# Kernel optimization log

Measured on AMD Instinct MI355X. Metric: run time of the kernel, lower is better.

Reference implementation:

```python
import jax, jax.numpy as jnp
import numpy as np

N, E, D, H, O = 50000, 800000, 128, 256, 64
BN_EPS = 1e-5


def setup_inputs() -> dict:
    key = jax.random.key(0)
    ks = jax.random.split(key, 12)
    x_indices = jnp.arange(N, dtype=jnp.int64) if jax.config.jax_enable_x64 else jnp.arange(N, dtype=jnp.int32)
    ei = jax.random.randint(ks[0], (2, E), 0, N, dtype=jnp.int32)
    s = lambda k, shape, fan: jax.random.normal(k, shape, dtype=jnp.float32) * (1.0 / np.sqrt(fan))
    return {
        "x_indices": x_indices,
        "ei": ei,
        "emb": jax.random.normal(ks[1], (N, D), dtype=jnp.float32),
        "W1": s(ks[2], (D, H), D), "b1": jnp.zeros((H,), jnp.float32),
        "g1": jnp.ones((H,), jnp.float32), "be1": jnp.zeros((H,), jnp.float32),
        "W2": s(ks[3], (H, H), H), "b2": jnp.zeros((H,), jnp.float32),
        "g2": jnp.ones((H,), jnp.float32), "be2": jnp.zeros((H,), jnp.float32),
        "W3": s(ks[4], (H, O), H), "b3": jnp.zeros((O,), jnp.float32),
    }


def reference(x_indices, ei, emb, W1, b1, g1, be1, W2, b2, g2, be2, W3, b3):
    n = emb.shape[0]
    # GCN normalization with self-loops (PyG GCNConv default):
    loop = jnp.arange(n, dtype=ei.dtype)
    row = jnp.concatenate([ei[0], loop])  # source
    col = jnp.concatenate([ei[1], loop])  # target (aggregation index)
    deg = jax.ops.segment_sum(jnp.ones_like(col, dtype=emb.dtype), col, num_segments=n)
    dinv = jnp.where(deg > 0, 1.0 / jnp.sqrt(jnp.maximum(deg, 1.0)), 0.0)
    norm = dinv[row] * dinv[col]  # [E+N]

    def conv(x, W, b):
        xl = x @ W                                   # [N, d_out]
        msg = xl[row] * norm[:, None]                # gather + scale
        return jax.ops.segment_sum(msg, col, num_segments=n) + b  # scatter-add

    def bn(x, g, be):  # batch-stat BatchNorm1d (training-mode stats)
        m = jnp.mean(x, axis=0)
        v = jnp.var(x, axis=0)
        return (x - m) * (g / jnp.sqrt(v + BN_EPS)) + be

    x = emb[x_indices]
    x = jax.nn.relu(bn(conv(x, W1, b1), g1, be1))
    x = jax.nn.relu(bn(conv(x, W2, b2), g2, be2))
    return conv(x, W3, b3)
```

## Files before the change

### kernel.cpp

```cpp
#include <hip/hip_runtime.h>
#include <hip/hip_bf16.h>

#define Dk 128
#define Hk 256
#define Ok 64
#define BN_EPS 1e-5f
#define NSLICE 8

typedef __attribute__((ext_vector_type(8))) short short8;
typedef __attribute__((ext_vector_type(4))) float f32x4;

static __device__ __forceinline__ float bf2f(ushort u) {
    union { uint32_t i; float f; } c; c.i = ((uint32_t)u) << 16; return c.f;
}
static __device__ __forceinline__ ushort f2bf(float f) {
    union { float f; uint32_t u; } c; c.f = f;
    return (ushort)((c.u + 0x7fffu + ((c.u >> 16) & 1u)) >> 16);
}


#define W1SZ (Dk * Hk)
#define W2SZ (Hk * Hk)
#define W3SZ (Hk * Ok)
#define WBLK ((W1SZ + W2SZ + W3SZ) / 256)
#define STATSP_FLOATS (2 * NSLICE * 512)

__global__ void count_cvt_kernel(const int* __restrict__ ecol, int* __restrict__ cnt, int E,
                                 const float* __restrict__ emb, const int* __restrict__ xidx,
                                 ushort* __restrict__ embb,
                                 const float* __restrict__ W1, const float* __restrict__ W2,
                                 const float* __restrict__ W3, ushort* __restrict__ W1t,
                                 ushort* __restrict__ W2t, ushort* __restrict__ W3t,
                                 float* __restrict__ statsP, int n) {
    const int cntBlocks = (E + 255) >> 8;
    const int embBlocks = (n * (Dk / 8) + 255) >> 8;
    int bid = blockIdx.x;
    if (bid < cntBlocks) {
        int e = bid * 256 + threadIdx.x;
        if (e < E) atomicAdd(&cnt[ecol[e]], 1);
        return;
    }
    bid -= cntBlocks;
    if (bid < embBlocks) {
        int gid = bid * 256 + threadIdx.x;
        int total = n * (Dk / 8);
        if (gid >= total) return;
        int node = gid >> 4, seg = gid & 15;
        int src = xidx[node];
        const float* p = &emb[(size_t)src * Dk + seg * 8];
        float4 lo = *(const float4*)p, hi = *(const float4*)(p + 4);
        ushort r[8] = {f2bf(lo.x), f2bf(lo.y), f2bf(lo.z), f2bf(lo.w),
                       f2bf(hi.x), f2bf(hi.y), f2bf(hi.z), f2bf(hi.w)};
        *(short8*)&embb[(size_t)gid * 8] = *(short8*)r;
        return;
    }
    bid -= embBlocks;
    if (bid < WBLK) {
        int gid = bid * 256 + threadIdx.x;
        if (gid < W1SZ) {
            int c = gid / Dk, k = gid - c * Dk;
            W1t[gid] = f2bf(W1[(size_t)k * Hk + c]);
        } else if (gid < W1SZ + W2SZ) {
            int idx = gid - W1SZ;
            int c = idx / Hk, k = idx - c * Hk;
            W2t[idx] = f2bf(W2[(size_t)k * Hk + c]);
        } else {
            int idx = gid - W1SZ - W2SZ;
            int c = idx / Hk, k = idx - c * Hk;
            W3t[idx] = f2bf(W3[(size_t)k * Ok + c]);
        }
        return;
    }
    bid -= WBLK;
    int idx = bid * 1024 + threadIdx.x * 4;
    if (idx < STATSP_FLOATS)
        *(float4*)&statsP[idx] = make_float4(0.f, 0.f, 0.f, 0.f);
}

__global__ void dinv_bsum_kernel(const int* __restrict__ cnt, float* __restrict__ dinv,
                                 int* __restrict__ fillc, int* __restrict__ bsum, int n) {
    __shared__ int sm[256];
    int i = blockIdx.x * 256 + threadIdx.x;
    int c = (i < n) ? cnt[i] : 0;
    if (i < n) { dinv[i] = rsqrtf((float)c + 1.0f); fillc[i] = 0; }
    sm[threadIdx.x] = c;
    __syncthreads();
    for (int s = 128; s; s >>= 1) {
        if (threadIdx.x < s) sm[threadIdx.x] += sm[threadIdx.x + s];
        __syncthreads();
    }
    if (!threadIdx.x) bsum[blockIdx.x] = sm[0];
}

__global__ void scan_off_kernel(const int* __restrict__ cnt, const int* __restrict__ bsum,
                                int* __restrict__ offv, int n) {
    __shared__ int sm[256];
    __shared__ int sbase;
    int t = threadIdx.x, bidx = blockIdx.x;
    int part = 0;
    for (int j = t; j < bidx; j += 256) part += bsum[j];
    sm[t] = part;
    __syncthreads();
    for (int s = 128; s; s >>= 1) {
        if (t < s) sm[t] += sm[t + s];
        __syncthreads();
    }
    if (t == 0) sbase = sm[0];
    __syncthreads();
    int base = sbase;
    __syncthreads();
    int i = bidx * 256 + t;
    int v = (i < n) ? cnt[i] : 0;
    sm[t] = v;
    __syncthreads();
    for (int s = 1; s < 256; s <<= 1) {
        int add = (t >= s) ? sm[t - s] : 0;
        __syncthreads();
        sm[t] += add;
        __syncthreads();
    }
    if (i < n) offv[i + 1] = base + sm[t];
    if (i == 0) offv[0] = 0;
}

__global__ void fill_kernel(const int* __restrict__ row, const int* __restrict__ col,
                            const int* __restrict__ off, int* __restrict__ fillc,
                            const float* __restrict__ dinv, int2* __restrict__ ep, int E) {
    int e = blockIdx.x * blockDim.x + threadIdx.x;
    if (e < E) {
        int c = col[e], r = row[e];
        int p = atomicAdd(&fillc[c], 1);
        ep[off[c] + p] = make_int2(r, __float_as_int(dinv[r]));
    }
}

__global__ void bn_finalize_kernel(const float* __restrict__ statsP, const float* __restrict__ g,
                                   const float* __restrict__ be, float* __restrict__ ss,
                                   float invn) {
    int f = threadIdx.x;
    float sum = 0.f, sq = 0.f;
    #pragma unroll
    for (int s = 0; s < NSLICE; ++s) {
        sum += statsP[s * 512 + f];
        sq  += statsP[s * 512 + 256 + f];
    }
    float mean = sum * invn;
    float var = sq * invn - mean * mean;
    float sc = g[f] * rsqrtf(var + BN_EPS);
    ss[f] = sc;
    ss[256 + f] = fmaf(-mean, sc, be[f]);
}


template<int KD, int BNT, bool STATS, bool BIAS, bool BN_A>
__global__ __launch_bounds__(256) void gemm128(
    const ushort* __restrict__ A, const ushort* __restrict__ Wt,
    ushort* __restrict__ Cout, int n, int Hout,
    const float* __restrict__ bias, float* __restrict__ statsP,
    const float* __restrict__ ss)
{
    constexpr int WN = (BNT == 128) ? 2 : 1;
    constexpr int MR = (BNT == 128) ? 4 : 2;
    constexpr int NR = 4;
    constexpr int TILE = (128 + BNT) * 32;
    constexpr int NT = KD / 32;
    __shared__ ushort lds[2 * TILE];
    __shared__ float ssc[BN_A ? KD : 1];
    __shared__ float ssh[BN_A ? KD : 1];

    const int tid = threadIdx.x;
    const int lane = tid & 63, wid = tid >> 6;
    const int wr = wid / WN, wc = wid % WN;
    const int lr = lane & 15, lg = lane >> 4;
    const int bm = blockIdx.x * 128;
    const int bn = blockIdx.y * BNT;

    if (BN_A) {
        for (int f = tid; f < KD; f += 256) {
            ssc[f] = ss[f];
            ssh[f] = ss[KD + f];
        }
        __syncthreads();
    }

    auto stage = [&](int buf, int k0) {
        ushort* As = lds + buf * TILE;
        ushort* Bs = As + 128 * 32;
        #pragma unroll
        for (int c = 0; c < 2; ++c) {
            int boff = wid * 2048 + c * 1024 + lane * 16;
            int row = boff >> 6;
            int k8 = (boff >> 4) & 3;
            int grow = bm + row; if (grow >= n) grow = n - 1;
            const ushort* src = &A[(size_t)grow * KD + k0 + k8 * 8];
            if (BN_A) {
                short8 av = *(const short8*)src;
                ushort r[8];
                #pragma unroll
                for (int j = 0; j < 8; ++j) {
                    int kf = k0 + k8 * 8 + j;
                    float v = bf2f((ushort)av[j]);
                    r[j] = f2bf(fmaxf(fmaf(v, ssc[kf], ssh[kf]), 0.f));
                }
                *(short8*)&As[row * 32 + k8 * 8] = *(short8*)r;
            } else {
                __builtin_amdgcn_global_load_lds(
                    (const __attribute__((address_space(1))) void*)src,
                    (__attribute__((address_space(3))) void*)&As[(wid * 2048 + c * 1024) >> 1],
                    16, 0, 0);
            }
        }
        constexpr int BC = BNT * 64 / 4096;
        #pragma unroll
        for (int c = 0; c < BC; ++c) {
            int boff = wid * (BNT * 16) + c * 1024 + lane * 16;
            int col = boff >> 6;
            int k8 = (boff >> 4) & 3;
            const ushort* src = &Wt[(size_t)(bn + col) * KD + k0 + k8 * 8];
            __builtin_amdgcn_global_load_lds(
                (const __attribute__((address_space(1))) void*)src,
                (__attribute__((address_space(3))) void*)&Bs[(wid * (BNT * 16) + c * 1024) >> 1],
                16, 0, 0);
        }
    };

    f32x4 acc[MR][NR] = {};

    stage(0, 0);
    __syncthreads();
    int cur = 0;
    for (int t = 0; t < NT; ++t) {
        if (t + 1 < NT) stage(cur ^ 1, (t + 1) * 32);
        ushort* As = lds + cur * TILE;
        ushort* Bs = As + 128 * 32;
        short8 af[MR], bfr[NR];
        #pragma unroll
        for (int m = 0; m < MR; ++m)
            af[m] = *(const short8*)&As[(wr * MR * 16 + m * 16 + lr) * 32 + lg * 8];
        #pragma unroll
        for (int nn = 0; nn < NR; ++nn)
            bfr[nn] = *(const short8*)&Bs[(wc * NR * 16 + nn * 16 + lr) * 32 + lg * 8];
        #pragma unroll
        for (int m = 0; m < MR; ++m)
            #pragma unroll
            for (int nn = 0; nn < NR; ++nn)
                acc[m][nn] = __builtin_amdgcn_mfma_f32_16x16x32_bf16(af[m], bfr[nn], acc[m][nn], 0, 0, 0);
        __syncthreads();
        cur ^= 1;
    }

    float s[NR], q[NR];
    #pragma unroll
    for (int nn = 0; nn < NR; ++nn) { s[nn] = 0.f; q[nn] = 0.f; }
    #pragma unroll
    for (int nn = 0; nn < NR; ++nn) {
        int col = bn + wc * NR * 16 + nn * 16 + lr;
        float bv = BIAS ? bias[col] : 0.f;
        #pragma unroll
        for (int m = 0; m < MR; ++m) {
            #pragma unroll
            for (int i = 0; i < 4; ++i) {
                int row = bm + wr * MR * 16 + m * 16 + lg * 4 + i;
                if (row < n) {
                    float v = acc[m][nn][i] + bv;
                    Cout[(size_t)row * Hout + col] = f2bf(v);
                    if (STATS) { s[nn] += v; q[nn] += v * v; }
                }
            }
        }
    }
    if (STATS) {
        float* sp = statsP + (size_t)(blockIdx.x & (NSLICE - 1)) * 2 * 256;
        #pragma unroll
        for (int nn = 0; nn < NR; ++nn) {
            s[nn] += __shfl_xor(s[nn], 16);
            q[nn] += __shfl_xor(q[nn], 16);
            s[nn] += __shfl_xor(s[nn], 32);
            q[nn] += __shfl_xor(q[nn], 32);
            if (lg == 0) {
                int col = bn + wc * NR * 16 + nn * 16 + lr;
                atomicAdd(&sp[col], s[nn]);
                atomicAdd(&sp[256 + col], q[nn]);
            }
        }
    }
}


template<int FH, int EPI, int MODE>
__global__ __launch_bounds__(256) void agg_kernel(
    const ushort* __restrict__ x, const int2* __restrict__ ep, const int* __restrict__ off,
    const float* __restrict__ dinv, const float* __restrict__ ss,
    const float* __restrict__ bias, void* __restrict__ outp, int n)
{
    constexpr int LPG = 64 / EPI;
    constexpr int VEC = FH / LPG;
    constexpr int U = 8 / EPI;
    const int tid = threadIdx.x;
    const int lane = tid & 63;
    const int wid = tid >> 6;
    const int node = blockIdx.x * 4 + wid;
    if (node >= n) return;
    const int grp = lane / LPG;
    const int flane = lane % LPG;
    const int fb = flane * VEC;
    const ushort* __restrict__ xb = x + fb;

    float sc[VEC], sh[VEC];
    if (MODE == 1) {
        float4 c4 = *(const float4*)&ss[fb];
        float4 h4 = *(const float4*)&ss[FH + fb];
        sc[0] = c4.x; sc[1] = c4.y; sc[2] = c4.z; sc[3] = c4.w;
        sh[0] = h4.x; sh[1] = h4.y; sh[2] = h4.z; sh[3] = h4.w;
    }
    auto xform = [&](ushort u, int v) -> float {
        float val = bf2f(u);
        if (MODE == 1) val = fmaxf(fmaf(val, sc[v], sh[v]), 0.f);
        return val;
    };

    float di = dinv[node];
    float acc[VEC] = {0.f, 0.f, 0.f, 0.f};
    if (EPI == 1 || grp == 0) {
        ushort4 t = *(const ushort4*)&xb[(size_t)node * FH];
        acc[0] = di * xform(t.x, 0); acc[1] = di * xform(t.y, 1);
        acc[2] = di * xform(t.z, 2); acc[3] = di * xform(t.w, 3);
    }
    const int e1 = off[node + 1];
    int b = off[node];
    for (; b + 8 <= e1; b += 8) {
        int2 p[U];
        ushort4 t[U];
        #pragma unroll
        for (int u = 0; u < U; ++u) p[u] = ep[b + grp + u * EPI];
        #pragma unroll
        for (int u = 0; u < U; ++u) t[u] = *(const ushort4*)&xb[(size_t)p[u].x * FH];
        #pragma unroll
        for (int u = 0; u < U; ++u) {
            float w = __int_as_float(p[u].y);
            acc[0] = fmaf(w, xform(t[u].x, 0), acc[0]);
            acc[1] = fmaf(w, xform(t[u].y, 1), acc[1]);
            acc[2] = fmaf(w, xform(t[u].z, 2), acc[2]);
            acc[3] = fmaf(w, xform(t[u].w, 3), acc[3]);
        }
    }
    if (b < e1) {
        #pragma unroll
        for (int u = 0; u < U; ++u) {
            int idx = b + grp + u * EPI;
            bool ok = idx < e1;
            int2 pp = ep[ok ? idx : b];
            ushort4 tt = *(const ushort4*)&xb[(size_t)pp.x * FH];
            float w = ok ? __int_as_float(pp.y) : 0.f;
            acc[0] = fmaf(w, xform(tt.x, 0), acc[0]);
            acc[1] = fmaf(w, xform(tt.y, 1), acc[1]);
            acc[2] = fmaf(w, xform(tt.z, 2), acc[2]);
            acc[3] = fmaf(w, xform(tt.w, 3), acc[3]);
        }
    }
    if (EPI == 4) {
        #pragma unroll
        for (int v = 0; v < VEC; ++v) acc[v] += __shfl_xor(acc[v], 16);
    }
    if (EPI >= 2) {
        #pragma unroll
        for (int v = 0; v < VEC; ++v) acc[v] += __shfl_xor(acc[v], 32);
    }
    if (grp == 0) {
        if (MODE == 2) {
            float4 bv = *(const float4*)&bias[fb];
            float4 res;
            res.x = fmaf(di, acc[0], bv.x); res.y = fmaf(di, acc[1], bv.y);
            res.z = fmaf(di, acc[2], bv.z); res.w = fmaf(di, acc[3], bv.w);
            *(float4*)((float*)outp + (size_t)node * FH + fb) = res;
        } else {
            ushort4 o;
            o.x = f2bf(di * acc[0]); o.y = f2bf(di * acc[1]);
            o.z = f2bf(di * acc[2]); o.w = f2bf(di * acc[3]);
            *(ushort4*)((ushort*)outp + (size_t)node * FH + fb) = o;
        }
    }
}


extern "C" void kernel_launch(void* const* d_in, const int* in_sizes, int n_in,
                              void* d_out, int out_size, void* d_ws, size_t ws_size,
                              hipStream_t stream) {
    const int*   x_idx = (const int*)d_in[0];
    const int*   ei    = (const int*)d_in[1];
    const float* emb   = (const float*)d_in[2];
    const float* W1    = (const float*)d_in[3];
    const float* b1    = (const float*)d_in[4];
    const float* g1    = (const float*)d_in[5];
    const float* be1   = (const float*)d_in[6];
    const float* W2    = (const float*)d_in[7];
    const float* b2    = (const float*)d_in[8];
    const float* g2    = (const float*)d_in[9];
    const float* be2   = (const float*)d_in[10];
    const float* W3    = (const float*)d_in[11];
    const float* b3    = (const float*)d_in[12];

    const int N = in_sizes[0];
    const int E = in_sizes[1] / 2;
    const int* erow = ei;
    const int* ecol = ei + E;

    char* p = (char*)d_ws;
    auto alloc = [&](size_t bytes) { char* q = p; p += (bytes + 255) & ~(size_t)255; return q; };
    const int nb = (N + 255) / 256;
    float*  dinv  = (float*) alloc((size_t)N * 4);
    int*    cnt   = (int*)   alloc((size_t)N * 4);
    int*    off   = (int*)   alloc((size_t)(N + 1) * 4);
    int*    fillc = (int*)   alloc((size_t)N * 4);
    int*    bsum  = (int*)   alloc((size_t)nb * 4);
    int2*   ep    = (int2*)  alloc((size_t)E * 8);
    float*  statsP= (float*) alloc((size_t)STATSP_FLOATS * 4);
    float*  stats1P = statsP, *stats2P = statsP + NSLICE * 512;
    float*  ss1   = (float*) alloc(512 * 4);
    float*  ss2   = (float*) alloc(512 * 4);
    ushort* W1t   = (ushort*)alloc((size_t)Dk * Hk * 2);
    ushort* W2t   = (ushort*)alloc((size_t)Hk * Hk * 2);
    ushort* W3t   = (ushort*)alloc((size_t)Hk * Ok * 2);
    ushort* bufU  = (ushort*)alloc((size_t)N * Hk * 2);
    ushort* embb  = bufU;
    ushort* agg1b = bufU + (size_t)N * Dk;
    ushort* conv2b= bufU;
    ushort* conv1b= (ushort*)alloc((size_t)N * Hk * 2);
    ushort* agg2b = (ushort*)alloc((size_t)N * Hk * 2);
    ushort* xl3b  = (ushort*)alloc((size_t)N * Ok * 2);

    const float invn = 1.0f / (float)N;

    hipMemsetAsync(cnt, 0, (size_t)N * 4, stream);
    const int cntBlocks = (E + 255) / 256;
    const int embBlocks = (N * (Dk / 8) + 255) / 256;
    count_cvt_kernel<<<cntBlocks + embBlocks + WBLK + (STATSP_FLOATS + 1023) / 1024,
                       256, 0, stream>>>(
        ecol, cnt, E, emb, x_idx, embb, W1, W2, W3, W1t, W2t, W3t, statsP, N);
    dinv_bsum_kernel<<<nb, 256, 0, stream>>>(cnt, dinv, fillc, bsum, N);
    scan_off_kernel<<<nb, 256, 0, stream>>>(cnt, bsum, off, N);
    fill_kernel<<<(E + 255) / 256, 256, 0, stream>>>(erow, ecol, off, fillc, dinv, ep, E);

    const int rb128 = (N + 127) / 128;
    const int aggBlocks = (N + 3) / 4;

    agg_kernel<Dk, 2, 0><<<aggBlocks, 256, 0, stream>>>(
        embb, ep, off, dinv, nullptr, nullptr, agg1b, N);
    gemm128<Dk, 128, true, true, false><<<dim3(rb128, Hk / 128), 256, 0, stream>>>(
        agg1b, W1t, conv1b, N, Hk, b1, stats1P, nullptr);
    bn_finalize_kernel<<<1, 256, 0, stream>>>(stats1P, g1, be1, ss1, invn);

    agg_kernel<Hk, 1, 1><<<aggBlocks, 256, 0, stream>>>(
        conv1b, ep, off, dinv, ss1, nullptr, agg2b, N);
    gemm128<Hk, 128, true, true, false><<<dim3(rb128, Hk / 128), 256, 0, stream>>>(
        agg2b, W2t, conv2b, N, Hk, b2, stats2P, nullptr);
    bn_finalize_kernel<<<1, 256, 0, stream>>>(stats2P, g2, be2, ss2, invn);

    gemm128<Hk, 64, false, false, true><<<dim3(rb128, 1), 256, 0, stream>>>(
        conv2b, W3t, xl3b, N, Ok, nullptr, nullptr, ss2);
    agg_kernel<Ok, 4, 2><<<aggBlocks, 256, 0, stream>>>(
        xl3b, ep, off, dinv, nullptr, b3, d_out, N);
}
```

Measured before the change: 300.5 us.

## Split BN statistics out of GEMM epilogue and tighten aggregation tail loop

Removes the per-block sum and sum-of-squares reduction and atomics from the GEMM epilogue, and computes BatchNorm statistics in a separate kernel that re-reads the bf16 conv output. This shrinks GEMM epilogue register pressure and atomic traffic, at the cost of an extra launch and a full extra read of the N×256 activation per layer. Statistics are now taken from bf16-rounded values rather than fp32 accumulators, which slightly changes numerics. The aggregation tail also replaces the masked 8-wide remainder with a 2×EPI unrolled loop plus a short masked loop, avoiding wasted gathers on nodes with few leftover edges.

```diff
diff --git a/kernel.cpp b/kernel.cpp
--- a/kernel.cpp
+++ b/kernel.cpp
@@ -134,6 +134,32 @@
     }
 }
 
+
+__global__ __launch_bounds__(256) void bn_stats_kernel(
+    const ushort* __restrict__ x, float* __restrict__ statsP, int n)
+{
+    __shared__ float red[8][256];
+    const int tid = threadIdx.x;
+    const int cg = tid & 63;
+    const int rg = tid >> 6;
+    const int c0 = cg * 4;
+    float s[4] = {0.f, 0.f, 0.f, 0.f}, q[4] = {0.f, 0.f, 0.f, 0.f};
+    for (int r = blockIdx.x * 4 + rg; r < n; r += gridDim.x * 4) {
+        ushort4 v = *(const ushort4*)&x[(size_t)r * Hk + c0];
+        float a0 = bf2f(v.x), a1 = bf2f(v.y), a2 = bf2f(v.z), a3 = bf2f(v.w);
+        s[0] += a0; s[1] += a1; s[2] += a2; s[3] += a3;
+        q[0] += a0 * a0; q[1] += a1 * a1; q[2] += a2 * a2; q[3] += a3 * a3;
+    }
+    #pragma unroll
+    for (int j = 0; j < 4; ++j) { red[rg][c0 + j] = s[j]; red[4 + rg][c0 + j] = q[j]; }
+    __syncthreads();
+    float ts = red[0][tid] + red[1][tid] + red[2][tid] + red[3][tid];
+    float tq = red[4][tid] + red[5][tid] + red[6][tid] + red[7][tid];
+    float* sp = statsP + (size_t)(blockIdx.x & (NSLICE - 1)) * 512;
+    atomicAdd(&sp[tid], ts);
+    atomicAdd(&sp[256 + tid], tq);
+}
+
 __global__ void bn_finalize_kernel(const float* __restrict__ statsP, const float* __restrict__ g,
                                    const float* __restrict__ be, float* __restrict__ ss,
                                    float invn) {
@@ -152,12 +178,11 @@
 }
 
 
-template<int KD, int BNT, bool STATS, bool BIAS, bool BN_A>
+template<int KD, int BNT, bool BIAS, bool BN_A>
 __global__ __launch_bounds__(256) void gemm128(
     const ushort* __restrict__ A, const ushort* __restrict__ Wt,
     ushort* __restrict__ Cout, int n, int Hout,
-    const float* __restrict__ bias, float* __restrict__ statsP,
-    const float* __restrict__ ss)
+    const float* __restrict__ bias, const float* __restrict__ ss)
 {
     constexpr int WN = (BNT == 128) ? 2 : 1;
     constexpr int MR = (BNT == 128) ? 4 : 2;
@@ -249,9 +274,6 @@
         cur ^= 1;
     }
 
-    float s[NR], q[NR];
-    #pragma unroll
-    for (int nn = 0; nn < NR; ++nn) { s[nn] = 0.f; q[nn] = 0.f; }
     #pragma unroll
     for (int nn = 0; nn < NR; ++nn) {
         int col = bn + wc * NR * 16 + nn * 16 + lr;
@@ -261,26 +283,8 @@
             #pragma unroll
             for (int i = 0; i < 4; ++i) {
                 int row = bm + wr * MR * 16 + m * 16 + lg * 4 + i;
-                if (row < n) {
-                    float v = acc[m][nn][i] + bv;
-                    Cout[(size_t)row * Hout + col] = f2bf(v);
-                    if (STATS) { s[nn] += v; q[nn] += v * v; }
-                }
-            }
-        }
-    }
-    if (STATS) {
-        float* sp = statsP + (size_t)(blockIdx.x & (NSLICE - 1)) * 2 * 256;
-        #pragma unroll
-        for (int nn = 0; nn < NR; ++nn) {
-            s[nn] += __shfl_xor(s[nn], 16);
-            q[nn] += __shfl_xor(q[nn], 16);
-            s[nn] += __shfl_xor(s[nn], 32);
-            q[nn] += __shfl_xor(q[nn], 32);
-            if (lg == 0) {
-                int col = bn + wc * NR * 16 + nn * 16 + lr;
-                atomicAdd(&sp[col], s[nn]);
-                atomicAdd(&sp[256 + col], q[nn]);
+                if (row < n)
+                    Cout[(size_t)row * Hout + col] = f2bf(acc[m][nn][i] + bv);
             }
         }
     }
@@ -344,19 +348,26 @@
             acc[3] = fmaf(w, xform(t[u].w, 3), acc[3]);
         }
     }
-    if (b < e1) {
-        #pragma unroll
-        for (int u = 0; u < U; ++u) {
-            int idx = b + grp + u * EPI;
-            bool ok = idx < e1;
-            int2 pp = ep[ok ? idx : b];
-            ushort4 tt = *(const ushort4*)&xb[(size_t)pp.x * FH];
-            float w = ok ? __int_as_float(pp.y) : 0.f;
-            acc[0] = fmaf(w, xform(tt.x, 0), acc[0]);
-            acc[1] = fmaf(w, xform(tt.y, 1), acc[1]);
-            acc[2] = fmaf(w, xform(tt.z, 2), acc[2]);
-            acc[3] = fmaf(w, xform(tt.w, 3), acc[3]);
-        }
+    if (EPI < 4) {
+        for (; b + 2 * EPI <= e1; b += 2 * EPI) {
+            int2 p0 = ep[b + grp], p1 = ep[b + grp + EPI];
+            ushort4 t0 = *(const ushort4*)&xb[(size_t)p0.x * FH];
+            ushort4 t1 = *(const ushort4*)&xb[(size_t)p1.x * FH];
+            float w0 = __int_as_float(p0.y), w1 = __int_as_float(p1.y);
+            acc[0] = fmaf(w0, xform(t0.x, 0), acc[0]); acc[1] = fmaf(w0, xform(t0.y, 1), acc[1]);
+            acc[2] = fmaf(w0, xform(t0.z, 2), acc[2]); acc[3] = fmaf(w0, xform(t0.w, 3), acc[3]);
+            acc[0] = fmaf(w1, xform(t1.x, 0), acc[0]); acc[1] = fmaf(w1, xform(t1.y, 1), acc[1]);
+            acc[2] = fmaf(w1, xform(t1.z, 2), acc[2]); acc[3] = fmaf(w1, xform(t1.w, 3), acc[3]);
+        }
+    }
+    for (; b < e1; b += EPI) {
+        int idx = b + grp;
+        bool ok = idx < e1;
+        int2 pp = ep[ok ? idx : e1 - 1];
+        ushort4 tt = *(const ushort4*)&xb[(size_t)pp.x * FH];
+        float w = ok ? __int_as_float(pp.y) : 0.f;
+        acc[0] = fmaf(w, xform(tt.x, 0), acc[0]); acc[1] = fmaf(w, xform(tt.y, 1), acc[1]);
+        acc[2] = fmaf(w, xform(tt.z, 2), acc[2]); acc[3] = fmaf(w, xform(tt.w, 3), acc[3]);
     }
     if (EPI == 4) {
         #pragma unroll
@@ -446,18 +457,20 @@
 
     agg_kernel<Dk, 2, 0><<<aggBlocks, 256, 0, stream>>>(
         embb, ep, off, dinv, nullptr, nullptr, agg1b, N);
-    gemm128<Dk, 128, true, true, false><<<dim3(rb128, Hk / 128), 256, 0, stream>>>(
-        agg1b, W1t, conv1b, N, Hk, b1, stats1P, nullptr);
+    gemm128<Dk, 128, true, false><<<dim3(rb128, Hk / 128), 256, 0, stream>>>(
+        agg1b, W1t, conv1b, N, Hk, b1, nullptr);
+    bn_stats_kernel<<<128, 256, 0, stream>>>(conv1b, stats1P, N);
     bn_finalize_kernel<<<1, 256, 0, stream>>>(stats1P, g1, be1, ss1, invn);
 
     agg_kernel<Hk, 1, 1><<<aggBlocks, 256, 0, stream>>>(
         conv1b, ep, off, dinv, ss1, nullptr, agg2b, N);
-    gemm128<Hk, 128, true, true, false><<<dim3(rb128, Hk / 128), 256, 0, stream>>>(
-        agg2b, W2t, conv2b, N, Hk, b2, stats2P, nullptr);
+    gemm128<Hk, 128, true, false><<<dim3(rb128, Hk / 128), 256, 0, stream>>>(
+        agg2b, W2t, conv2b, N, Hk, b2, nullptr);
+    bn_stats_kernel<<<128, 256, 0, stream>>>(conv2b, stats2P, N);
     bn_finalize_kernel<<<1, 256, 0, stream>>>(stats2P, g2, be2, ss2, invn);
 
-    gemm128<Hk, 64, false, false, true><<<dim3(rb128, 1), 256, 0, stream>>>(
-        conv2b, W3t, xl3b, N, Ok, nullptr, nullptr, ss2);
+    gemm128<Hk, 64, false, true><<<dim3(rb128, 1), 256, 0, stream>>>(
+        conv2b, W3t, xl3b, N, Ok, nullptr, ss2);
     agg_kernel<Ok, 4, 2><<<aggBlocks, 256, 0, stream>>>(
         xl3b, ep, off, dinv, nullptr, b3, d_out, N);
 }
```

New measurement: 338.6 us. +12.7%, slower.
